# Kernel tuning notes

Measured on AMD Instinct MI355X. Metric: run time of the kernel, lower is better.

## Reference

```python
import jax, jax.numpy as jnp
import numpy as np

D_EMB = 128
N_CLASSES = 10
ITEM_DIM = 64


def _mlp(x, w1, b1, w2, b2):
    # torch nn.GELU default is exact (erf) gelu
    return jax.nn.gelu(x @ w1 + b1, approximate=False) @ w2 + b2


def sparsemax(z, axis=-1):
    """Euclidean projection of logits onto the probability simplex (sparsemax)."""
    n = z.shape[axis]
    z_sorted = -jnp.sort(-z, axis=axis)                      # descending
    ks = jnp.arange(1, n + 1, dtype=z.dtype)
    csum = jnp.cumsum(z_sorted, axis=axis)
    support = (1.0 + ks * z_sorted) > csum                   # broadcast over last axis
    k_z = jnp.sum(support, axis=axis, keepdims=True)         # support size
    csum_k = jnp.take_along_axis(csum, k_z.astype(jnp.int32) - 1, axis=axis)
    tau = (csum_k - 1.0) / k_z.astype(z.dtype)
    return jnp.maximum(z - tau, 0.0)


def setup_inputs() -> dict:
    key = jax.random.key(0)
    ks = jax.random.split(key, 22)
    d = D_EMB

    def lin(k, fan_in, fan_out):
        lim = (1.0 / fan_in) ** 0.5
        kw, kb = jax.random.split(k)
        w = jax.random.uniform(kw, (fan_in, fan_out), jnp.float32, -lim, lim)
        b = jax.random.uniform(kb, (fan_out,), jnp.float32, -lim, lim)
        return w, b

    wx1, bx1 = lin(ks[0], ITEM_DIM, d)
    wx2, bx2 = lin(ks[1], d, d)
    wq1, bq1 = lin(ks[2], 1, d)
    wq2, bq2 = lin(ks[3], d, d)
    wqp, bqp = lin(ks[4], d, d)
    wkp, bkp = lin(ks[5], d, d)
    wvp, bvp = lin(ks[6], d, d)
    wp1, bp1 = lin(ks[7], d, d)
    wp2, bp2 = lin(ks[8], d, N_CLASSES)

    x_items = jax.random.normal(ks[9], (32, 16384, ITEM_DIM), jnp.float32)
    x_query = jax.random.normal(ks[10], (32, 1), jnp.float32)
    return {
        "x_items": x_items, "x_query": x_query,
        "wx1": wx1, "bx1": bx1, "wx2": wx2, "bx2": bx2,
        "wq1": wq1, "bq1": bq1, "wq2": wq2, "bq2": bq2,
        "wqp": wqp, "bqp": bqp, "wkp": wkp, "bkp": bkp,
        "wvp": wvp, "bvp": bvp, "wp1": wp1, "bp1": bp1,
        "wp2": wp2, "bp2": bp2,
    }


def reference(x_items, x_query, wx1, bx1, wx2, bx2, wq1, bq1, wq2, bq2,
              wqp, bqp, wkp, bkp, wvp, bvp, wp1, bp1, wp2, bp2):
    # x_items: [B, N, item_dim]; x_query: [B, 1] -> unsqueeze(-1) -> [B, 1, 1]
    h_items = _mlp(x_items, wx1, bx1, wx2, bx2)              # [B, N, d]
    h_query = _mlp(x_query[..., None], wq1, bq1, wq2, bq2)   # [B, 1, d]
    q = h_query @ wqp + bqp                                   # [B, 1, d]
    k = h_items @ wkp + bkp                                   # [B, N, d]
    v = h_items @ wvp + bvp                                   # [B, N, d]
    scale = k.shape[-1] ** -0.5
    scores = jnp.einsum('bqd,bnd->bqn', q, k) * scale         # [B, 1, N]
    attn = sparsemax(scores, axis=-1)                         # simplex mapping
    z = jnp.einsum('bqn,bnd->bqd', attn, v)[:, 0]             # squeeze(1) -> [B, d]
    return _mlp(z, wp1, bp1, wp2, bp2)                        # [B, n_classes]
```

## Files before the change

### kernel.cpp

```cpp
#include <hip/hip_runtime.h>
#include <hip/hip_bf16.h>
#include <cstdint>

#define BATCH 32
#define NITEMS 16384
#define DEMB 128
#define IDIM 64

typedef short short8 __attribute__((ext_vector_type(8)));
typedef float f32x4 __attribute__((ext_vector_type(4)));

__device__ inline unsigned short f2bf(float f) {
    union { float f; unsigned int u; } v; v.f = f;
    unsigned int u = v.u;
    unsigned int r = (u + 0x7FFFu + ((u >> 16) & 1u)) >> 16;
    return (unsigned short)r;
}
__device__ inline float bf2f(unsigned short h) {
    union { unsigned int u; float f; } v; v.u = ((unsigned int)h) << 16;
    return v.f;
}

__device__ inline float erf_approx(float x) {
    float ax = fabsf(x);
    float t = __builtin_amdgcn_rcpf(fmaf(0.3275911f, ax, 1.0f));
    float p = fmaf(1.061405429f, t, -1.453152027f);
    p = fmaf(p, t, 1.421413741f);
    p = fmaf(p, t, -0.284496736f);
    p = fmaf(p, t, 0.254829592f);
    p = p * t;
    float e = __expf(-ax * ax);
    float r = fmaf(-p, e, 1.0f);
    return copysignf(r, x);
}
__device__ inline float gelu_f(float v) {
    return 0.5f * v * (1.0f + erf_approx(v * 0.70710678118654752f));
}

__global__ __launch_bounds__(128) void k0_prep(
    const float* __restrict__ xq, const float* __restrict__ wq1, const float* __restrict__ bq1,
    const float* __restrict__ wq2, const float* __restrict__ bq2,
    const float* __restrict__ wqp, const float* __restrict__ bqp,
    const float* __restrict__ wkp,
    const float* __restrict__ wx1, const float* __restrict__ wx2,
    float* __restrict__ r_out, unsigned short* __restrict__ w1h, unsigned short* __restrict__ w1l) {
    __shared__ float buf1[128], buf2[128], buf3[128], buf4[128];
    int t = threadIdx.x;
    int blk = blockIdx.x;
    if (blk < BATCH) {
        int b = blk;
        float xqv = xq[b];
        buf1[t] = gelu_f(fmaf(xqv, wq1[t], bq1[t]));
        __syncthreads();
        float acc = bq2[t];
        for (int j = 0; j < 128; j++) acc = fmaf(buf1[j], wq2[j * 128 + t], acc);
        buf2[t] = acc;
        __syncthreads();
        acc = bqp[t];
        for (int j = 0; j < 128; j++) acc = fmaf(buf2[j], wqp[j * 128 + t], acc);
        buf3[t] = acc;
        __syncthreads();
        acc = 0.f;
        for (int i = 0; i < 128; i++) acc = fmaf(wkp[t * 128 + i], buf3[i], acc);
        buf4[t] = acc * 0.08838834764831845f;
        __syncthreads();
        acc = 0.f;
        for (int i = 0; i < 128; i++) acc = fmaf(wx2[t * 128 + i], buf4[i], acc);
        r_out[b * 128 + t] = acc;
    } else {
        for (int idx = t; idx < 64 * 128; idx += 128) {
            int k = idx >> 7, n = idx & 127;
            float v = wx1[idx];
            unsigned short hi = f2bf(v);
            float lo = v - bf2f(hi);
            w1h[n * 64 + k] = hi;
            w1l[n * 64 + k] = f2bf(lo);
        }
    }
}

__global__ __launch_bounds__(256) void k1_items(
    const float* __restrict__ x, const unsigned short* __restrict__ w1h,
    const unsigned short* __restrict__ w1l, const float* __restrict__ bx1,
    const float* __restrict__ r_in, float* __restrict__ scores) {
    __shared__ alignas(16) unsigned short lxh[64 * 72];
    __shared__ alignas(16) unsigned short lxl[64 * 72];
    __shared__ float red[4][64];
    int tid = threadIdx.x;
    int wave = tid >> 6, lane = tid & 63;
    int quad = lane >> 4, l15 = lane & 15;
    int tile = blockIdx.x;
    long item0 = (long)tile * 64;
    int b = tile >> 8;

    short8 bh[2][2], bl[2][2];
    {
        int nb = wave * 32 + l15;
        for (int s = 0; s < 2; s++)
            for (int nt = 0; nt < 2; nt++) {
                int off = (nb + nt * 16) * 64 + s * 32 + quad * 8;
                bh[s][nt] = *(const short8*)(w1h + off);
                bl[s][nt] = *(const short8*)(w1l + off);
            }
    }
    float bias[2], rv[2];
    for (int nt = 0; nt < 2; nt++) {
        int c = wave * 32 + nt * 16 + l15;
        bias[nt] = bx1[c];
        rv[nt] = r_in[b * 128 + c];
    }

    const float* xg = x + item0 * 64;
    for (int p = 0; p < 4; p++) {
        int idx = tid + p * 256;
        int row = idx >> 4, c4 = (idx & 15) * 4;
        float4 v = *(const float4*)(xg + row * 64 + c4);
        unsigned int ux = __float_as_uint(v.x), uy = __float_as_uint(v.y);
        unsigned int uz = __float_as_uint(v.z), uw = __float_as_uint(v.w);
        unsigned int hi01 = __builtin_amdgcn_perm(uy, ux, 0x07060302u);
        unsigned int hi23 = __builtin_amdgcn_perm(uw, uz, 0x07060302u);
        float lx = v.x - __uint_as_float(ux & 0xFFFF0000u);
        float ly = v.y - __uint_as_float(uy & 0xFFFF0000u);
        float lz = v.z - __uint_as_float(uz & 0xFFFF0000u);
        float lw = v.w - __uint_as_float(uw & 0xFFFF0000u);
        unsigned int lo01 = __builtin_amdgcn_perm(__float_as_uint(ly), __float_as_uint(lx), 0x07060302u);
        unsigned int lo23 = __builtin_amdgcn_perm(__float_as_uint(lw), __float_as_uint(lz), 0x07060302u);
        *(uint2*)(lxh + row * 72 + c4) = make_uint2(hi01, hi23);
        *(uint2*)(lxl + row * 72 + c4) = make_uint2(lo01, lo23);
    }
    __syncthreads();

    f32x4 acc[4][2];
    for (int mt = 0; mt < 4; mt++) for (int nt = 0; nt < 2; nt++) acc[mt][nt] = (f32x4)0.f;

    for (int s = 0; s < 2; s++) {
        int koff = s * 32 + quad * 8;
        short8 ah[4], al[4];
        for (int mt = 0; mt < 4; mt++) {
            int rb = (mt * 16 + l15) * 72 + koff;
            ah[mt] = *(const short8*)(lxh + rb);
            al[mt] = *(const short8*)(lxl + rb);
        }
        for (int mt = 0; mt < 4; mt++)
            for (int nt = 0; nt < 2; nt++) {
                acc[mt][nt] = __builtin_amdgcn_mfma_f32_16x16x32_bf16(al[mt], bh[s][nt], acc[mt][nt], 0, 0, 0);
                acc[mt][nt] = __builtin_amdgcn_mfma_f32_16x16x32_bf16(ah[mt], bl[s][nt], acc[mt][nt], 0, 0, 0);
                acc[mt][nt] = __builtin_amdgcn_mfma_f32_16x16x32_bf16(ah[mt], bh[s][nt], acc[mt][nt], 0, 0, 0);
            }
    }

    float pr[4][4];
    for (int mt = 0; mt < 4; mt++) for (int rr = 0; rr < 4; rr++) pr[mt][rr] = 0.f;
    for (int mt = 0; mt < 4; mt++)
        for (int nt = 0; nt < 2; nt++)
            for (int rr = 0; rr < 4; rr++) {
                float g = gelu_f(acc[mt][nt][rr] + bias[nt]);
                pr[mt][rr] = fmaf(g, rv[nt], pr[mt][rr]);
            }
    for (int off = 1; off < 16; off <<= 1)
        for (int mt = 0; mt < 4; mt++)
            for (int rr = 0; rr < 4; rr++)
                pr[mt][rr] += __shfl_xor(pr[mt][rr], off);
    if (l15 == 0)
        for (int mt = 0; mt < 4; mt++)
            for (int rr = 0; rr < 4; rr++)
                red[wave][mt * 16 + quad * 4 + rr] = pr[mt][rr];
    __syncthreads();
    if (tid < 64)
        scores[item0 + tid] = red[0][tid] + red[1][tid] + red[2][tid] + red[3][tid];
}

__global__ __launch_bounds__(1024) void k2_tau(const float* __restrict__ scores,
                                               float* __restrict__ tau_out,
                                               float* __restrict__ u) {
    __shared__ float la[2][16], lc[2][16];
    int b = blockIdx.x, t = threadIdx.x;
    int wid = t >> 6, lane = t & 63;
    const float* s = scores + (size_t)b * NITEMS;
    float z[16];
    for (int i = 0; i < 16; i++) z[i] = s[t + i * 1024];
    float sm = 0.f;
    for (int i = 0; i < 16; i++) sm += z[i];
    for (int off = 32; off; off >>= 1) sm += __shfl_xor(sm, off);
    if (lane == 0) la[1][wid] = sm;
    __syncthreads();
    float tot = 0.f;
    for (int i = 0; i < 16; i++) tot += la[1][i];
    float tau = (tot - 1.0f) * (1.0f / 16384.0f);
    for (int it = 0; it < 20; it++) {
        int pb = it & 1;
        float ls = 0.f, ct = 0.f;
        for (int i = 0; i < 16; i++) {
            bool a = z[i] > tau;
            ls += a ? z[i] : 0.f;
            ct += a ? 1.f : 0.f;
        }
        for (int off = 32; off; off >>= 1) {
            ls += __shfl_xor(ls, off);
            ct += __shfl_xor(ct, off);
        }
        if (lane == 0) { la[pb][wid] = ls; lc[pb][wid] = ct; }
        __syncthreads();
        float tls = 0.f, tct = 0.f;
        for (int i = 0; i < 16; i++) { tls += la[pb][i]; tct += lc[pb][i]; }
        tau = (tls - 1.0f) / tct;
    }
    if (t == 0) tau_out[b] = tau;
    if (t < 128) u[b * 128 + t] = 0.f;
}

__global__ __launch_bounds__(256) void k3_support(
    const float* __restrict__ scores, const float* __restrict__ tau_in,
    const float* __restrict__ x,
    const float* __restrict__ wx1, const float* __restrict__ bx1,
    const float* __restrict__ wx2, const float* __restrict__ bx2,
    float* __restrict__ u) {
    __shared__ float red[4][128];
    int blk = blockIdx.x;
    int b = blk >> 5;
    int sub = blk & 31;
    int wave = threadIdx.x >> 6, lane = threadIdx.x & 63;
    int wslot = sub * 4 + wave;
    int base = wslot * 128;
    float tau = tau_in[b];
    int t0 = lane, t1 = lane + 64;
    float bb0 = bx1[t0], bb1 = bx1[t1];
    float cc0 = bx2[t0], cc1 = bx2[t1];
    float u0 = 0.f, u1 = 0.f;
    const float* srow = scores + (size_t)b * NITEMS + base;
    for (int half = 0; half < 2; half++) {
        float sv = srow[half * 64 + lane] - tau;
        unsigned long long mask = __ballot(sv > 0.f);
        while (mask) {
            int src = __ffsll((long long)mask) - 1;
            mask &= mask - 1;
            float wgt = __shfl(sv, src);
            int item = base + half * 64 + src;
            const float* xr = x + ((size_t)b * NITEMS + item) * 64;
            float xv = xr[lane];
            float p0 = bb0, p1 = bb1;
            for (int k = 0; k < 64; k++) {
                float xk = __shfl(xv, k);
                p0 = fmaf(xk, wx1[k * 128 + t0], p0);
                p1 = fmaf(xk, wx1[k * 128 + t1], p1);
            }
            float h0 = gelu_f(p0), h1 = gelu_f(p1);
            float a0 = cc0, a1 = cc1;
            for (int j = 0; j < 64; j++) {
                float hj = __shfl(h0, j);
                a0 = fmaf(hj, wx2[j * 128 + t0], a0);
                a1 = fmaf(hj, wx2[j * 128 + t1], a1);
            }
            for (int j = 0; j < 64; j++) {
                float hj = __shfl(h1, j);
                a0 = fmaf(hj, wx2[(j + 64) * 128 + t0], a0);
                a1 = fmaf(hj, wx2[(j + 64) * 128 + t1], a1);
            }
            u0 = fmaf(wgt, a0, u0);
            u1 = fmaf(wgt, a1, u1);
        }
    }
    red[wave][t0] = u0;
    red[wave][t1] = u1;
    __syncthreads();
    if (threadIdx.x < 128) {
        float s = red[0][threadIdx.x] + red[1][threadIdx.x] +
                  red[2][threadIdx.x] + red[3][threadIdx.x];
        atomicAdd(&u[b * 128 + threadIdx.x], s);
    }
}

__global__ __launch_bounds__(128) void k4_head(
    const float* __restrict__ u, const float* __restrict__ wvp, const float* __restrict__ bvp,
    const float* __restrict__ wp1, const float* __restrict__ bp1,
    const float* __restrict__ wp2, const float* __restrict__ bp2,
    float* __restrict__ out) {
    __shared__ float ub[128], zb[128], tb[128];
    int b = blockIdx.x, t = threadIdx.x;
    ub[t] = u[b * 128 + t];
    __syncthreads();
    float z = bvp[t];
    for (int j = 0; j < 128; j++) z = fmaf(ub[j], wvp[j * 128 + t], z);
    zb[t] = z;
    __syncthreads();
    float h = bp1[t];
    for (int j = 0; j < 128; j++) h = fmaf(zb[j], wp1[j * 128 + t], h);
    tb[t] = gelu_f(h);
    __syncthreads();
    if (t < 10) {
        float o = bp2[t];
        for (int j = 0; j < 128; j++) o = fmaf(tb[j], wp2[j * 10 + t], o);
        out[b * 10 + t] = o;
    }
}

extern "C" void kernel_launch(void* const* d_in, const int* in_sizes, int n_in,
                              void* d_out, int out_size, void* d_ws, size_t ws_size,
                              hipStream_t stream) {
    const float* x_items = (const float*)d_in[0];
    const float* x_query = (const float*)d_in[1];
    const float* wx1 = (const float*)d_in[2];
    const float* bx1 = (const float*)d_in[3];
    const float* wx2 = (const float*)d_in[4];
    const float* bx2 = (const float*)d_in[5];
    const float* wq1 = (const float*)d_in[6];
    const float* bq1 = (const float*)d_in[7];
    const float* wq2 = (const float*)d_in[8];
    const float* bq2 = (const float*)d_in[9];
    const float* wqp = (const float*)d_in[10];
    const float* bqp = (const float*)d_in[11];
    const float* wkp = (const float*)d_in[12];
    const float* wvp = (const float*)d_in[14];
    const float* bvp = (const float*)d_in[15];
    const float* wp1 = (const float*)d_in[16];
    const float* bp1 = (const float*)d_in[17];
    const float* wp2 = (const float*)d_in[18];
    const float* bp2 = (const float*)d_in[19];
    float* out = (float*)d_out;

    char* ws = (char*)d_ws;
    float* r_buf        = (float*)(ws);
    unsigned short* w1h = (unsigned short*)(ws + 16384);
    unsigned short* w1l = (unsigned short*)(ws + 32768);
    float* scores       = (float*)(ws + 49152);
    float* tau          = (float*)(ws + 49152 + 2097152);
    float* u            = (float*)(ws + 49152 + 2097152 + 256);

    k0_prep<<<33, 128, 0, stream>>>(x_query, wq1, bq1, wq2, bq2, wqp, bqp, wkp,
                                    wx1, wx2, r_buf, w1h, w1l);
    k1_items<<<(BATCH * NITEMS) / 64, 256, 0, stream>>>(x_items, w1h, w1l, bx1, r_buf, scores);
    k2_tau<<<BATCH, 1024, 0, stream>>>(scores, tau, u);
    k3_support<<<BATCH * 32, 256, 0, stream>>>(scores, tau, x_items, wx1, bx1, wx2, bx2, u);
    k4_head<<<BATCH, 128, 0, stream>>>(u, wvp, bvp, wp1, bp1, wp2, bp2, out);
}
```

Baseline: 338.3 us.

## Process four item tiles per block with double-buffered LDS prefetch and cheaper GELU

Each k1 block now handles 256 items as four 64-item tiles. The next tile's global loads are issued before the current tile's MFMA work and are staged into a second LDS buffer, so memory latency overlaps compute and the per-block weight loads are amortised. GELU is also rewritten as a rational erfc approximation (a degree-6 polynomial raised to the 16th power, then one reciprocal) instead of the exp-based erf. The cost is a 4x smaller grid, double the LDS footprint and more registers, and the new GELU has different accuracy characteristics.

```diff
diff --git a/kernel.cpp b/kernel.cpp
--- a/kernel.cpp
+++ b/kernel.cpp
@@ -21,20 +21,21 @@
     return v.f;
 }
 
-__device__ inline float erf_approx(float x) {
-    float ax = fabsf(x);
-    float t = __builtin_amdgcn_rcpf(fmaf(0.3275911f, ax, 1.0f));
-    float p = fmaf(1.061405429f, t, -1.453152027f);
-    p = fmaf(p, t, 1.421413741f);
-    p = fmaf(p, t, -0.284496736f);
-    p = fmaf(p, t, 0.254829592f);
-    p = p * t;
-    float e = __expf(-ax * ax);
-    float r = fmaf(-p, e, 1.0f);
-    return copysignf(r, x);
-}
-__device__ inline float gelu_f(float v) {
-    return 0.5f * v * (1.0f + erf_approx(v * 0.70710678118654752f));
+__device__ inline float gelu_f(float x) {
+    float y = fabsf(x) * 0.70710678118654752f;
+    float d = fmaf(y, 0.0000430638f, 0.0002765672f);
+    d = fmaf(d, y, 0.0001520143f);
+    d = fmaf(d, y, 0.0092705272f);
+    d = fmaf(d, y, 0.0422820123f);
+    d = fmaf(d, y, 0.0705230784f);
+    d = fmaf(d, y, 1.0f);
+    float s = d * d;
+    s = s * s;
+    s = s * s;
+    s = s * s;
+    float pe = 0.5f * __builtin_amdgcn_rcpf(s);
+    float phi = (x > 0.f) ? (1.0f - pe) : pe;
+    return x * phi;
 }
 
 __global__ __launch_bounds__(128) void k0_prep(
@@ -79,19 +80,38 @@
     }
 }
 
+__device__ inline void stage_tile(const float4* v, unsigned short* dh, unsigned short* dl,
+                                  const int* srow, const int* sc4) {
+    for (int p = 0; p < 4; p++) {
+        float4 w = v[p];
+        unsigned int ux = __float_as_uint(w.x), uy = __float_as_uint(w.y);
+        unsigned int uz = __float_as_uint(w.z), uw = __float_as_uint(w.w);
+        unsigned int hi01 = __builtin_amdgcn_perm(uy, ux, 0x07060302u);
+        unsigned int hi23 = __builtin_amdgcn_perm(uw, uz, 0x07060302u);
+        float lx = w.x - __uint_as_float(ux & 0xFFFF0000u);
+        float ly = w.y - __uint_as_float(uy & 0xFFFF0000u);
+        float lz = w.z - __uint_as_float(uz & 0xFFFF0000u);
+        float lw = w.w - __uint_as_float(uw & 0xFFFF0000u);
+        unsigned int lo01 = __builtin_amdgcn_perm(__float_as_uint(ly), __float_as_uint(lx), 0x07060302u);
+        unsigned int lo23 = __builtin_amdgcn_perm(__float_as_uint(lw), __float_as_uint(lz), 0x07060302u);
+        *(uint2*)(dh + srow[p] * 72 + sc4[p]) = make_uint2(hi01, hi23);
+        *(uint2*)(dl + srow[p] * 72 + sc4[p]) = make_uint2(lo01, lo23);
+    }
+}
+
 __global__ __launch_bounds__(256) void k1_items(
     const float* __restrict__ x, const unsigned short* __restrict__ w1h,
     const unsigned short* __restrict__ w1l, const float* __restrict__ bx1,
     const float* __restrict__ r_in, float* __restrict__ scores) {
-    __shared__ alignas(16) unsigned short lxh[64 * 72];
-    __shared__ alignas(16) unsigned short lxl[64 * 72];
-    __shared__ float red[4][64];
+    __shared__ alignas(16) unsigned short lxh[2][64 * 72];
+    __shared__ alignas(16) unsigned short lxl[2][64 * 72];
+    __shared__ float red[2][4][64];
     int tid = threadIdx.x;
     int wave = tid >> 6, lane = tid & 63;
     int quad = lane >> 4, l15 = lane & 15;
-    int tile = blockIdx.x;
-    long item0 = (long)tile * 64;
-    int b = tile >> 8;
+    int blk = blockIdx.x;
+    int b = blk >> 6;
+    const float* xg = x + (size_t)blk * 256 * 64;
 
     short8 bh[2][2], bl[2][2];
     {
@@ -110,64 +130,73 @@
         rv[nt] = r_in[b * 128 + c];
     }
 
-    const float* xg = x + item0 * 64;
+    int srow[4], sc4[4];
     for (int p = 0; p < 4; p++) {
         int idx = tid + p * 256;
-        int row = idx >> 4, c4 = (idx & 15) * 4;
-        float4 v = *(const float4*)(xg + row * 64 + c4);
-        unsigned int ux = __float_as_uint(v.x), uy = __float_as_uint(v.y);
-        unsigned int uz = __float_as_uint(v.z), uw = __float_as_uint(v.w);
-        unsigned int hi01 = __builtin_amdgcn_perm(uy, ux, 0x07060302u);
-        unsigned int hi23 = __builtin_amdgcn_perm(uw, uz, 0x07060302u);
-        float lx = v.x - __uint_as_float(ux & 0xFFFF0000u);
-        float ly = v.y - __uint_as_float(uy & 0xFFFF0000u);
-        float lz = v.z - __uint_as_float(uz & 0xFFFF0000u);
-        float lw = v.w - __uint_as_float(uw & 0xFFFF0000u);
-        unsigned int lo01 = __builtin_amdgcn_perm(__float_as_uint(ly), __float_as_uint(lx), 0x07060302u);
-        unsigned int lo23 = __builtin_amdgcn_perm(__float_as_uint(lw), __float_as_uint(lz), 0x07060302u);
-        *(uint2*)(lxh + row * 72 + c4) = make_uint2(hi01, hi23);
-        *(uint2*)(lxl + row * 72 + c4) = make_uint2(lo01, lo23);
-    }
-    __syncthreads();
-
-    f32x4 acc[4][2];
-    for (int mt = 0; mt < 4; mt++) for (int nt = 0; nt < 2; nt++) acc[mt][nt] = (f32x4)0.f;
-
-    for (int s = 0; s < 2; s++) {
-        int koff = s * 32 + quad * 8;
-        short8 ah[4], al[4];
-        for (int mt = 0; mt < 4; mt++) {
-            int rb = (mt * 16 + l15) * 72 + koff;
-            ah[mt] = *(const short8*)(lxh + rb);
-            al[mt] = *(const short8*)(lxl + rb);
-        }
+        srow[p] = idx >> 4;
+        sc4[p] = (idx & 15) * 4;
+    }
+
+    float4 v[4];
+    for (int p = 0; p < 4; p++)
+        v[p] = *(const float4*)(xg + srow[p] * 64 + sc4[p]);
+    stage_tile(v, lxh[0], lxl[0], srow, sc4);
+    __syncthreads();
+
+    for (int t = 0; t < 4; t++) {
+        int pb = t & 1;
+        if (t < 3) {
+            const float* xt = xg + (t + 1) * 4096;
+            for (int p = 0; p < 4; p++)
+                v[p] = *(const float4*)(xt + srow[p] * 64 + sc4[p]);
+        }
+
+        f32x4 acc[4][2];
+        for (int mt = 0; mt < 4; mt++) for (int nt = 0; nt < 2; nt++) acc[mt][nt] = (f32x4)0.f;
+        const unsigned short* bufh = lxh[pb];
+        const unsigned short* bufl = lxl[pb];
+        for (int s = 0; s < 2; s++) {
+            int koff = s * 32 + quad * 8;
+            short8 ah[4], al[4];
+            for (int mt = 0; mt < 4; mt++) {
+                int rb = (mt * 16 + l15) * 72 + koff;
+                ah[mt] = *(const short8*)(bufh + rb);
+                al[mt] = *(const short8*)(bufl + rb);
+            }
+            for (int mt = 0; mt < 4; mt++)
+                for (int nt = 0; nt < 2; nt++) {
+                    acc[mt][nt] = __builtin_amdgcn_mfma_f32_16x16x32_bf16(al[mt], bh[s][nt], acc[mt][nt], 0, 0, 0);
+                    acc[mt][nt] = __builtin_amdgcn_mfma_f32_16x16x32_bf16(ah[mt], bl[s][nt], acc[mt][nt], 0, 0, 0);
+                    acc[mt][nt] = __builtin_amdgcn_mfma_f32_16x16x32_bf16(ah[mt], bh[s][nt], acc[mt][nt], 0, 0, 0);
+                }
+        }
+
+        float pr[4][4];
+        for (int mt = 0; mt < 4; mt++) for (int rr = 0; rr < 4; rr++) pr[mt][rr] = 0.f;
         for (int mt = 0; mt < 4; mt++)
-            for (int nt = 0; nt < 2; nt++) {
-                acc[mt][nt] = __builtin_amdgcn_mfma_f32_16x16x32_bf16(al[mt], bh[s][nt], acc[mt][nt], 0, 0, 0);
-                acc[mt][nt] = __builtin_amdgcn_mfma_f32_16x16x32_bf16(ah[mt], bl[s][nt], acc[mt][nt], 0, 0, 0);
-                acc[mt][nt] = __builtin_amdgcn_mfma_f32_16x16x32_bf16(ah[mt], bh[s][nt], acc[mt][nt], 0, 0, 0);
-            }
-    }
-
-    float pr[4][4];
-    for (int mt = 0; mt < 4; mt++) for (int rr = 0; rr < 4; rr++) pr[mt][rr] = 0.f;
-    for (int mt = 0; mt < 4; mt++)
-        for (int nt = 0; nt < 2; nt++)
-            for (int rr = 0; rr < 4; rr++) {
-                float g = gelu_f(acc[mt][nt][rr] + bias[nt]);
-                pr[mt][rr] = fmaf(g, rv[nt], pr[mt][rr]);
-            }
-    for (int off = 1; off < 16; off <<= 1)
-        for (int mt = 0; mt < 4; mt++)
-            for (int rr = 0; rr < 4; rr++)
-                pr[mt][rr] += __shfl_xor(pr[mt][rr], off);
-    if (l15 == 0)
-        for (int mt = 0; mt < 4; mt++)
-            for (int rr = 0; rr < 4; rr++)
-                red[wave][mt * 16 + quad * 4 + rr] = pr[mt][rr];
-    __syncthreads();
-    if (tid < 64)
-        scores[item0 + tid] = red[0][tid] + red[1][tid] + red[2][tid] + red[3][tid];
+            for (int nt = 0; nt < 2; nt++)
+                for (int rr = 0; rr < 4; rr++) {
+                    float g = gelu_f(acc[mt][nt][rr] + bias[nt]);
+                    pr[mt][rr] = fmaf(g, rv[nt], pr[mt][rr]);
+                }
+        for (int off = 1; off < 16; off <<= 1)
+            for (int mt = 0; mt < 4; mt++)
+                for (int rr = 0; rr < 4; rr++)
+                    pr[mt][rr] += __shfl_xor(pr[mt][rr], off);
+        if (l15 == 0)
+            for (int mt = 0; mt < 4; mt++)
+                for (int rr = 0; rr < 4; rr++)
+                    red[pb][wave][mt * 16 + quad * 4 + rr] = pr[mt][rr];
+
+        if (t < 3)
+            stage_tile(v, lxh[1 - pb], lxl[1 - pb], srow, sc4);
+
+        __syncthreads();
+
+        if (tid < 64)
+            scores[(size_t)blk * 256 + t * 64 + tid] =
+                red[pb][0][tid] + red[pb][1][tid] + red[pb][2][tid] + red[pb][3][tid];
+    }
 }
 
 __global__ __launch_bounds__(1024) void k2_tau(const float* __restrict__ scores,
@@ -328,7 +357,7 @@
 
     k0_prep<<<33, 128, 0, stream>>>(x_query, wq1, bq1, wq2, bq2, wqp, bqp, wkp,
                                     wx1, wx2, r_buf, w1h, w1l);
-    k1_items<<<(BATCH * NITEMS) / 64, 256, 0, stream>>>(x_items, w1h, w1l, bx1, r_buf, scores);
+    k1_items<<<(BATCH * NITEMS) / 256, 256, 0, stream>>>(x_items, w1h, w1l, bx1, r_buf, scores);
     k2_tau<<<BATCH, 1024, 0, stream>>>(scores, tau, u);
     k3_support<<<BATCH * 32, 256, 0, stream>>>(scores, tau, x_items, wx1, bx1, wx2, bx2, u);
     k4_head<<<BATCH, 128, 0, stream>>>(u, wvp, bvp, wp1, bp1, wp2, bp2, out);
```

Result: no change. 334.3 us (-1.2%).
